# Optimization experiments

Hardware: AMD Instinct MI355X
Metric: run time of the kernel (lower is better)

## Reference

```python
import jax, jax.numpy as jnp
import numpy as np

L, B, C = 512, 64, 512  # seq_len, batch, tags_size


def setup_inputs() -> dict:
    key = jax.random.key(0)
    k1, k2, k3, k4, k5, k6 = jax.random.split(key, 6)
    std = (1.0 / C) ** 0.5
    emit = jax.random.normal(k1, (L, B, C), dtype=jnp.float32)
    trans = jax.random.normal(k2, (C, C), dtype=jnp.float32) * std
    trans_from_start = jax.random.normal(k3, (C,), dtype=jnp.float32) * std
    trans_to_end = jax.random.normal(k4, (C,), dtype=jnp.float32) * std
    target = jax.random.randint(k5, (L, B), 0, C)
    # left-aligned length mask so mask.sum(0)-1 indexes the last valid step
    lens = jax.random.randint(k6, (B,), L // 2, L + 1)
    mask = jnp.arange(L)[:, None] < lens[None, :]
    return {"emit": emit, "target": target, "mask": mask, "trans": trans,
            "trans_from_start": trans_from_start, "trans_to_end": trans_to_end}


def _log_z(emit, mask, trans, trans_from_start, trans_to_end):
    log_alpha0 = emit[0] + trans_from_start  # (B, C)

    def step(log_alpha, xs):
        e_i, m_i = xs  # (B, C), (B,)
        # scores[b, j] = logsumexp_i( log_alpha[b, i] + trans[i, j] + e_i[b, j] )
        s = jax.nn.logsumexp(log_alpha[:, :, None] + trans[None, :, :] + e_i[:, None, :], axis=1)
        log_alpha = jnp.where(m_i[:, None], s, log_alpha)
        return log_alpha, None

    log_alpha, _ = jax.lax.scan(step, log_alpha0, (emit[1:], mask[1:]))
    return jax.nn.logsumexp(log_alpha + trans_to_end, axis=1).sum()


def _score(emit, target, mask, trans, trans_from_start, trans_to_end):
    l, b, c = emit.shape
    tr = trans[target[:-1], target[1:]]  # (L-1, B)
    scores = jnp.concatenate([jnp.zeros((1, b), emit.dtype), tr], axis=0)
    scores = scores + jnp.take_along_axis(emit, target[:, :, None], axis=2)[..., 0]
    score = jnp.where(mask, scores, jnp.zeros((), emit.dtype)).sum()
    ends = mask.sum(axis=0) - 1  # (B,) index of last valid step
    last_tags = target[ends, jnp.arange(b)]
    score = score + trans_from_start[target[0]].sum() + trans_to_end[last_tags].sum()
    return score


def reference(emit, target, mask, trans, trans_from_start, trans_to_end):
    b = emit.shape[1]
    log_z = _log_z(emit, mask, trans, trans_from_start, trans_to_end)
    score = _score(emit, target, mask, trans, trans_from_start, trans_to_end)
    return (log_z - score) / b
```

## Files before the change

### kernel.cpp

```cpp
#include <hip/hip_runtime.h>
#include <hip/hip_bf16.h>
#include <stdint.h>

#define LL 512
#define BB 64
#define CC 512
#define TM 255

typedef float float4v __attribute__((ext_vector_type(4)));
typedef int   int4v   __attribute__((ext_vector_type(4)));
typedef int   int8v   __attribute__((ext_vector_type(8)));

#define WS_ET     262144
#define WS_SCORE  524288
#define WS_SVA    524292
#define WS_SVB    524548
#define WS_ALPHA  528384
#define WS_BETA   659456


__device__ __forceinline__ bool mask_at(const void* maskp, bool is_byte, int t, int b) {
    if (is_byte) return ((const unsigned char*)maskp)[t * BB + b] != 0;
    return ((const int*)maskp)[t * BB + b] != 0;
}

__device__ __forceinline__ float rowmax16_dpp(float x) {
    int t;
    t = __builtin_amdgcn_update_dpp(0, __float_as_int(x), 0x128, 0xF, 0xF, true);
    x = fmaxf(x, __int_as_float(t));
    t = __builtin_amdgcn_update_dpp(0, __float_as_int(x), 0x124, 0xF, 0xF, true);
    x = fmaxf(x, __int_as_float(t));
    t = __builtin_amdgcn_update_dpp(0, __float_as_int(x), 0x122, 0xF, 0xF, true);
    x = fmaxf(x, __int_as_float(t));
    t = __builtin_amdgcn_update_dpp(0, __float_as_int(x), 0x121, 0xF, 0xF, true);
    x = fmaxf(x, __int_as_float(t));
    return x;
}

__device__ __forceinline__ float4v vmax4(float4v a, float4v b) {
    float4v r;
    r[0] = fmaxf(a[0], b[0]); r[1] = fmaxf(a[1], b[1]);
    r[2] = fmaxf(a[2], b[2]); r[3] = fmaxf(a[3], b[3]);
    return r;
}
__device__ __forceinline__ float4v vmin4s(float4v a, float c) {
    float4v r;
    r[0] = fminf(a[0], c); r[1] = fminf(a[1], c);
    r[2] = fminf(a[2], c); r[3] = fminf(a[3], c);
    return r;
}

__device__ __forceinline__ void step_barrier() {
    asm volatile("s_waitcnt lgkmcnt(0)" ::: "memory");
    __builtin_amdgcn_sched_barrier(0);
    __builtin_amdgcn_s_barrier();
    asm volatile("" ::: "memory");
}

__global__ void prep_kernel(const float* __restrict__ trans, unsigned char* __restrict__ ws) {
    int g = blockIdx.x * blockDim.x + threadIdx.x;
    if (g == 0) *(float*)(ws + WS_SCORE) = 0.0f;
    if (g >= 512 * 128) return;
    int n  = g & 511;
    int pd = g >> 9;
    int wv = pd >> 4, rw = pd & 15;
    float f[4], ft[4];
#pragma unroll
    for (int nt = 0; nt < 4; ++nt) {
        int k = 64 * wv + 16 * nt + rw;
        f[nt]  = __expf(trans[(size_t)k * CC + n]);
        ft[nt] = __expf(trans[(size_t)n * CC + k]);
    }
    int r = 0;
    r = __builtin_amdgcn_cvt_pk_fp8_f32(f[0], f[1], r, false);
    r = __builtin_amdgcn_cvt_pk_fp8_f32(f[2], f[3], r, true);
    ((int*)ws)[n * 128 + pd] = r;
    int r2 = 0;
    r2 = __builtin_amdgcn_cvt_pk_fp8_f32(ft[0], ft[1], r2, false);
    r2 = __builtin_amdgcn_cvt_pk_fp8_f32(ft[2], ft[3], r2, true);
    ((int*)(ws + WS_ET))[n * 128 + pd] = r2;
}

__launch_bounds__(512, 2)
__global__ void crf_scan_kernel(const float* __restrict__ emit,
                                const int* __restrict__ target,
                                const void* __restrict__ maskp,
                                const float* __restrict__ trans,
                                const float* __restrict__ tfs,
                                const float* __restrict__ t2e,
                                unsigned char* __restrict__ ws) {
    const int tid = threadIdx.x;
    const bool is_byte = ((const unsigned char*)maskp)[1] != 0;

    if (blockIdx.x >= 8) {
        int sb = blockIdx.x - 8;
        float val = 0.0f;
        for (int e = sb * 512 + tid; e < LL * BB; e += 32 * 512) {
            int t = e >> 6, b = e & 63;
            if (mask_at(maskp, is_byte, t, b)) {
                int tg  = target[t * BB + b];
                float v = emit[(size_t)(t * BB + b) * CC + tg];
                if (t > 0) v += trans[(size_t)target[(t - 1) * BB + b] * CC + tg];
                val += v;
            }
        }
        if (sb == 0 && tid < BB) {
            int b = tid;
            val += tfs[target[b]];
            int lo = 0, hi = LL;
            while (lo < hi) {
                int mid = (lo + hi) >> 1;
                if (mask_at(maskp, is_byte, mid, b)) lo = mid + 1; else hi = mid;
            }
            val += t2e[target[(lo - 1) * BB + b]];
        }
        for (int off = 32; off > 0; off >>= 1) val += __shfl_down(val, off);
        if ((tid & 63) == 0) atomicAdd((float*)(ws + WS_SCORE), val);
        return;
    }

    const bool is_fwd = blockIdx.x < 4;
    const int B0 = (is_fwd ? blockIdx.x : blockIdx.x - 4) * 16;

    __shared__ __align__(16) unsigned char p8[2][16 * 528];
    __shared__ __align__(16) float mslot[4][16];
    __shared__ float m0S[16];
    __shared__ float red[16][32];
    __shared__ int   lenS[16];
    __shared__ float mInitS;

    const int wv   = tid >> 6;
    const int lane = tid & 63;
    const int q    = lane >> 4;
    const int r15  = lane & 15;

    const unsigned char* ews = ws + (is_fwd ? 0 : WS_ET);
    int8v ef[4][4];
#pragma unroll
    for (int nt = 0; nt < 4; ++nt) {
        int n = (wv * 4 + nt) * 16 + r15;
#pragma unroll
        for (int kk4 = 0; kk4 < 4; ++kk4) {
            const unsigned char* src = ews + n * 512 + kk4 * 128 + q * 32;
            int4v lo = *(const int4v*)(src);
            int4v hi = *(const int4v*)(src + 16);
            ef[nt][kk4] = __builtin_shufflevector(lo, hi, 0, 1, 2, 3, 4, 5, 6, 7);
        }
    }

    const int c5 = tid >> 5;
    const int s5 = tid & 31;

    if (is_fwd) {
        {
            float lmax = -3.0e38f;
#pragma unroll
            for (int i = 0; i < 4; ++i) {
                int j4 = s5 + 32 * i;
                float4v em = *(const float4v*)(emit + (size_t)(B0 + c5) * CC + 4 * j4);
                float4v tf = *(const float4v*)(tfs + 4 * j4);
                float4v a = em + tf;
                lmax = fmaxf(lmax, fmaxf(fmaxf(a.x, a.y), fmaxf(a.z, a.w)));
            }
            red[c5][s5] = lmax;
        }
        __syncthreads();
        if (tid < 16) {
            float m0 = red[tid][0];
            for (int s = 1; s < 32; ++s) m0 = fmaxf(m0, red[tid][s]);
            m0S[tid] = m0;
            mslot[0][tid] = 1.0f;
            mslot[1][tid] = 0.0f;
            mslot[2][tid] = 0.0f;
            mslot[3][tid] = 0.0f;
        }
        __syncthreads();
        {
            float m0 = m0S[c5];
#pragma unroll
            for (int i = 0; i < 4; ++i) {
                int pd = s5 + 32 * i;
                int wvv = pd >> 4, rw = pd & 15;
                float f[4];
#pragma unroll
                for (int nt = 0; nt < 4; ++nt) {
                    int k = 64 * wvv + 16 * nt + rw;
                    f[nt] = __expf(emit[(size_t)(B0 + c5) * CC + k] + tfs[k] - m0);
                }
                int r = 0;
                r = __builtin_amdgcn_cvt_pk_fp8_f32(f[0], f[1], r, false);
                r = __builtin_amdgcn_cvt_pk_fp8_f32(f[2], f[3], r, true);
                *(int*)(&p8[0][0] + c5 * 528 + pd * 4) = r;
            }
        }
        __syncthreads();
    } else {
        {
            float m = t2e[tid];
            for (int off = 32; off > 0; off >>= 1) m = fmaxf(m, __shfl_xor(m, off));
            if (lane == 0) ((float*)red)[wv] = m;
        }
        if (tid < 16) {
            mslot[0][tid] = 0.0f;
            mslot[1][tid] = 0.0f;
            mslot[2][tid] = 0.0f;
            mslot[3][tid] = 0.0f;
        }
        __syncthreads();
        if (tid == 0) {
            float m = ((float*)red)[0];
            for (int i = 1; i < 8; ++i) m = fmaxf(m, ((float*)red)[i]);
            mInitS = __expf(m);
        }
        __syncthreads();
        {
#pragma unroll
            for (int i = 0; i < 4; ++i) {
                int pd = s5 + 32 * i;
                int wvv = pd >> 4, rw = pd & 15;
                float f[4];
#pragma unroll
                for (int nt = 0; nt < 4; ++nt)
                    f[nt] = __expf(t2e[64 * wvv + 16 * nt + rw]);
                int r = 0;
                r = __builtin_amdgcn_cvt_pk_fp8_f32(f[0], f[1], r, false);
                r = __builtin_amdgcn_cvt_pk_fp8_f32(f[2], f[3], r, true);
                *(int*)(&p8[0][0] + c5 * 528 + pd * 4) = r;
                *(int*)(&p8[1][0] + c5 * 528 + pd * 4) = r;
            }
            int part = 0;
            for (int k = 0; k < 16; ++k)
                part += mask_at(maskp, is_byte, s5 * 16 + k, B0 + c5) ? 1 : 0;
            red[c5][s5] = (float)part;
        }
        __syncthreads();
        if (tid < 16) {
            int s = 0;
            for (int i = 0; i < 32; ++i) s += (int)red[tid][i];
            lenS[tid] = s;
        }
        __syncthreads();
    }

    int4v gsum = {0, 0, 0, 0};
    const float4v z4 = {0.f, 0.f, 0.f, 0.f};

    if (is_fwd) {
        const float* eb0 = emit + (size_t)(BB + B0 + q * 4) * CC + (wv * 64 + r15);
        const float* eb1 = eb0 + 2 * CC;
        float4v ex4[4];
#pragma unroll
        for (int nt = 0; nt < 4; ++nt) {
            ex4[nt][0] = __expf(eb0[0 * CC + nt * 16]);
            ex4[nt][1] = __expf(eb0[1 * CC + nt * 16]);
            ex4[nt][2] = __expf(eb1[0 * CC + nt * 16]);
            ex4[nt][3] = __expf(eb1[1 * CC + nt * 16]);
        }

#pragma unroll 2
        for (int t = 1; t <= TM; ++t) {
            const int wp = t & 1;
            const int rp = wp ^ 1;
            eb0 += BB * CC;
            eb1 += BB * CC;

            const unsigned char* pr = &p8[rp][0] + r15 * 528 + q * 32;
            int8v af[4];
#pragma unroll
            for (int kk4 = 0; kk4 < 4; ++kk4) {
                int4v lo = *(const int4v*)(pr + kk4 * 128);
                int4v hi = *(const int4v*)(pr + kk4 * 128 + 16);
                af[kk4] = __builtin_shufflevector(lo, hi, 0, 1, 2, 3, 4, 5, 6, 7);
            }
            int4v me = *(const int4v*)&mslot[(t - 1) & 3][q * 4];

            float4v emn4[4];
#pragma unroll
            for (int nt = 0; nt < 4; ++nt) {
                emn4[nt][0] = eb0[0 * CC + nt * 16];
                emn4[nt][1] = eb0[1 * CC + nt * 16];
                emn4[nt][2] = eb1[0 * CC + nt * 16];
                emn4[nt][3] = eb1[1 * CC + nt * 16];
            }

            int4v e4 = me >> 23;
            int4v s2b = (248 - e4) << 23;
            float4v s24;
            s24[0] = __int_as_float(s2b[0]); s24[1] = __int_as_float(s2b[1]);
            s24[2] = __int_as_float(s2b[2]); s24[3] = __int_as_float(s2b[3]);

            if (wv == 0 && r15 == 0)
                *(float4v*)&mslot[(t + 1) & 3][q * 4] = z4;

            float4v acc[4];
#pragma unroll
            for (int nt = 0; nt < 4; ++nt) acc[nt] = z4;

#pragma unroll
            for (int kk4 = 0; kk4 < 4; ++kk4)
#pragma unroll
                for (int nt = 0; nt < 2; ++nt)
                    acc[nt] = __builtin_amdgcn_mfma_scale_f32_16x16x128_f8f6f4(
                        af[kk4], ef[nt][kk4], acc[nt],
                        0, 0, 0, 0x7F7F7F7F, 0, 0x7F7F7F7F);

            float4v exn4[4];
#pragma unroll
            for (int nt = 0; nt < 4; ++nt) {
                exn4[nt][0] = __expf(emn4[nt][0]);
                exn4[nt][1] = __expf(emn4[nt][1]);
                exn4[nt][2] = __expf(emn4[nt][2]);
                exn4[nt][3] = __expf(emn4[nt][3]);
            }

#pragma unroll
            for (int kk4 = 0; kk4 < 4; ++kk4)
#pragma unroll
                for (int nt = 2; nt < 4; ++nt)
                    acc[nt] = __builtin_amdgcn_mfma_scale_f32_16x16x128_f8f6f4(
                        af[kk4], ef[nt][kk4], acc[nt],
                        0, 0, 0, 0x7F7F7F7F, 0, 0x7F7F7F7F);

            float4v p4[4];
#pragma unroll
            for (int nt = 0; nt < 4; ++nt) {
                float4v exr = ex4[nt] * s24;
                p4[nt] = acc[nt] * exr;
            }

            if (t == TM) {
                float* wA = (float*)(ws + WS_ALPHA) + (size_t)(B0 + q * 4) * CC + (wv * 64 + r15);
#pragma unroll
                for (int nt = 0; nt < 4; ++nt)
#pragma unroll
                    for (int rr = 0; rr < 4; ++rr)
                        wA[(size_t)rr * CC + nt * 16] = p4[nt][rr];
            }

            float4v rm4 = vmax4(vmax4(p4[0], p4[1]), vmax4(p4[2], p4[3]));
#pragma unroll
            for (int rr = 0; rr < 4; ++rr) {
                float mr = rowmax16_dpp(rm4[rr]);
                if (r15 == 0)
                    atomicMax((int*)&mslot[t & 3][q * 4 + rr], __float_as_int(mr));
            }

            {
                unsigned char* wrow = &p8[wp][0] + (wv * 16 + r15) * 4;
                float4v pc[4];
#pragma unroll
                for (int nt = 0; nt < 4; ++nt) pc[nt] = vmin4s(p4[nt], 448.0f);
#pragma unroll
                for (int rr = 0; rr < 4; ++rr) {
                    int r = 0;
                    r = __builtin_amdgcn_cvt_pk_fp8_f32(pc[0][rr], pc[1][rr], r, false);
                    r = __builtin_amdgcn_cvt_pk_fp8_f32(pc[2][rr], pc[3][rr], r, true);
                    *(int*)(wrow + (q * 4 + rr) * 528) = r;
                }
            }

            if (wv == 0 && r15 == 0) gsum += (e4 - 121);

#pragma unroll
            for (int nt = 0; nt < 4; ++nt) ex4[nt] = exn4[nt];
            step_barrier();
        }
        if (wv == 0 && r15 == 0) {
#pragma unroll
            for (int rr = 0; rr < 4; ++rr)
                ((float*)(ws + WS_SVA))[B0 + q * 4 + rr] =
                    m0S[q * 4 + rr] + 0.6931471805599453f * (float)gsum[rr];
        }
    } else {
        int lenR[4];
#pragma unroll
        for (int rr = 0; rr < 4; ++rr) lenR[rr] = lenS[q * 4 + rr];
        const int eInit = __float_as_int(mInitS) >> 23;

        const float* eb0 = emit + ((size_t)(LL - 1) * BB + B0 + q * 4) * CC + (wv * 64 + r15);
        const float* eb1 = eb0 + 2 * CC;
        float4v ex4[4];
#pragma unroll
        for (int nt = 0; nt < 4; ++nt) {
            ex4[nt][0] = __expf(eb0[0 * CC + nt * 16]);
            ex4[nt][1] = __expf(eb0[1 * CC + nt * 16]);
            ex4[nt][2] = __expf(eb1[0 * CC + nt * 16]);
            ex4[nt][3] = __expf(eb1[1 * CC + nt * 16]);
        }

#pragma unroll 2
        for (int it = 0; it < 256; ++it) {
            const int t  = 510 - it;
            const int wp = it & 1;
            const int rp = wp ^ 1;
            eb0 -= BB * CC;
            eb1 -= BB * CC;

            const unsigned char* pr = &p8[rp][0] + r15 * 528 + q * 32;
            int8v af[4];
#pragma unroll
            for (int kk4 = 0; kk4 < 4; ++kk4) {
                int4v lo = *(const int4v*)(pr + kk4 * 128);
                int4v hi = *(const int4v*)(pr + kk4 * 128 + 16);
                af[kk4] = __builtin_shufflevector(lo, hi, 0, 1, 2, 3, 4, 5, 6, 7);
            }
            int4v me = *(const int4v*)&mslot[(it + 3) & 3][q * 4];

            float4v emn4[4];
#pragma unroll
            for (int nt = 0; nt < 4; ++nt) {
                emn4[nt][0] = eb0[0 * CC + nt * 16];
                emn4[nt][1] = eb0[1 * CC + nt * 16];
                emn4[nt][2] = eb1[0 * CC + nt * 16];
                emn4[nt][3] = eb1[1 * CC + nt * 16];
            }

            int4v e4 = me >> 23;
            int4v eU;
            float4v s2U;
#pragma unroll
            for (int rr = 0; rr < 4; ++rr) {
                bool ui = (t >= lenR[rr] - 2);
                int e = ui ? eInit : e4[rr];
                eU[rr] = e;
                s2U[rr] = __int_as_float((248 - e) << 23);
            }

            if (wv == 0 && r15 == 0)
                *(float4v*)&mslot[(it + 1) & 3][q * 4] = z4;

            float4v acc[4];
#pragma unroll
            for (int nt = 0; nt < 4; ++nt) acc[nt] = z4;

#pragma unroll
            for (int kk4 = 0; kk4 < 4; ++kk4)
#pragma unroll
                for (int nt = 0; nt < 2; ++nt)
                    acc[nt] = __builtin_amdgcn_mfma_scale_f32_16x16x128_f8f6f4(
                        af[kk4], ef[nt][kk4], acc[nt],
                        0, 0, 0, 0x7F7F7F7F, 0, 0x7F7F7F7F);

            float4v exn4[4];
#pragma unroll
            for (int nt = 0; nt < 4; ++nt) {
                exn4[nt][0] = __expf(emn4[nt][0]);
                exn4[nt][1] = __expf(emn4[nt][1]);
                exn4[nt][2] = __expf(emn4[nt][2]);
                exn4[nt][3] = __expf(emn4[nt][3]);
            }

#pragma unroll
            for (int kk4 = 0; kk4 < 4; ++kk4)
#pragma unroll
                for (int nt = 2; nt < 4; ++nt)
                    acc[nt] = __builtin_amdgcn_mfma_scale_f32_16x16x128_f8f6f4(
                        af[kk4], ef[nt][kk4], acc[nt],
                        0, 0, 0, 0x7F7F7F7F, 0, 0x7F7F7F7F);

            float4v p4[4];
#pragma unroll
            for (int nt = 0; nt < 4; ++nt) {
                float4v exr = ex4[nt] * s2U;
                p4[nt] = acc[nt] * exr;
            }

            if (t == TM) {
                float* wB = (float*)(ws + WS_BETA) + (size_t)(B0 + q * 4) * CC + (wv * 64 + r15);
#pragma unroll
                for (int nt = 0; nt < 4; ++nt) {
                    float e2 = __expf(t2e[wv * 64 + nt * 16 + r15]);
#pragma unroll
                    for (int rr = 0; rr < 4; ++rr)
                        wB[(size_t)rr * CC + nt * 16] = (t <= lenR[rr] - 2) ? p4[nt][rr] : e2;
                }
            }

            float4v rm4 = vmax4(vmax4(p4[0], p4[1]), vmax4(p4[2], p4[3]));
#pragma unroll
            for (int rr = 0; rr < 4; ++rr) {
                float mr = rowmax16_dpp(rm4[rr]);
                if (r15 == 0)
                    atomicMax((int*)&mslot[it & 3][q * 4 + rr], __float_as_int(mr));
            }

            {
                unsigned char* wrow = &p8[wp][0] + (wv * 16 + r15) * 4;
                float4v pc[4];
#pragma unroll
                for (int nt = 0; nt < 4; ++nt) pc[nt] = vmin4s(p4[nt], 448.0f);
#pragma unroll
                for (int rr = 0; rr < 4; ++rr) {
                    int r = 0;
                    r = __builtin_amdgcn_cvt_pk_fp8_f32(pc[0][rr], pc[1][rr], r, false);
                    r = __builtin_amdgcn_cvt_pk_fp8_f32(pc[2][rr], pc[3][rr], r, true);
                    if (t <= lenR[rr] - 2)
                        *(int*)(wrow + (q * 4 + rr) * 528) = r;
                }
            }

            if (wv == 0 && r15 == 0) {
#pragma unroll
                for (int rr = 0; rr < 4; ++rr)
                    if (t <= lenR[rr] - 2) gsum[rr] += (eU[rr] - 121);
            }

#pragma unroll
            for (int nt = 0; nt < 4; ++nt) ex4[nt] = exn4[nt];
            step_barrier();
        }
        if (wv == 0 && r15 == 0) {
#pragma unroll
            for (int rr = 0; rr < 4; ++rr)
                ((float*)(ws + WS_SVB))[B0 + q * 4 + rr] =
                    0.6931471805599453f * (float)gsum[rr];
        }
    }
}

__global__ void combine_kernel(const unsigned char* __restrict__ ws, float* __restrict__ out) {
    __shared__ float acc8[8];
    const int tid = threadIdx.x;
    const int c  = tid >> 3;
    const int s8 = tid & 7;
    const float* A = (const float*)(ws + WS_ALPHA) + (size_t)c * CC;
    const float* B = (const float*)(ws + WS_BETA)  + (size_t)c * CC;
    float d = 0.0f;
    for (int i = s8; i < CC; i += 8) d += A[i] * B[i];
    d += __shfl_xor(d, 1);
    d += __shfl_xor(d, 2);
    d += __shfl_xor(d, 4);
    float v = 0.0f;
    if (s8 == 0)
        v = ((const float*)(ws + WS_SVA))[c] + ((const float*)(ws + WS_SVB))[c] + __logf(d);
    for (int off = 32; off > 0; off >>= 1) v += __shfl_down(v, off);
    if ((tid & 63) == 0) acc8[tid >> 6] = v;
    __syncthreads();
    if (tid == 0) {
        float s = 0.0f;
        for (int i = 0; i < 8; ++i) s += acc8[i];
        out[0] = (s - *(const float*)(ws + WS_SCORE)) * (1.0f / 64.0f);
    }
}

extern "C" void kernel_launch(void* const* d_in, const int* in_sizes, int n_in,
                              void* d_out, int out_size, void* d_ws, size_t ws_size,
                              hipStream_t stream) {
    const float* emit   = (const float*)d_in[0];
    const int*   target = (const int*)d_in[1];
    const void*  maskp  = d_in[2];
    const float* trans  = (const float*)d_in[3];
    const float* tfs    = (const float*)d_in[4];
    const float* t2e    = (const float*)d_in[5];
    unsigned char* ws   = (unsigned char*)d_ws;
    float* out          = (float*)d_out;

    prep_kernel<<<256, 256, 0, stream>>>(trans, ws);
    crf_scan_kernel<<<40, 512, 0, stream>>>(emit, target, maskp, trans, tfs, t2e, ws);
    combine_kernel<<<1, 512, 0, stream>>>(ws, out);
}
```

Measured before the change: 495.4 us.

## Fuse trans prep into scan kernel and interleave MFMA halves with epilogue

```diff
diff --git a/kernel.cpp b/kernel.cpp
--- a/kernel.cpp
+++ b/kernel.cpp
@@ -11,13 +11,16 @@
 typedef int   int4v   __attribute__((ext_vector_type(4)));
 typedef int   int8v   __attribute__((ext_vector_type(8)));
 
-#define WS_ET     262144
-#define WS_SCORE  524288
-#define WS_SVA    524292
-#define WS_SVB    524548
+#define WS_SPART  524288
+#define WS_SVA    524416
+#define WS_SVB    524672
 #define WS_ALPHA  528384
 #define WS_BETA   659456
 
+
+__device__ __forceinline__ int kperm(int p) {
+    return 64 * (p >> 6) + 16 * (p & 3) + ((p >> 2) & 15);
+}
 
 __device__ __forceinline__ bool mask_at(const void* maskp, bool is_byte, int t, int b) {
     if (is_byte) return ((const unsigned char*)maskp)[t * BB + b] != 0;
@@ -37,48 +40,11 @@
     return x;
 }
 
-__device__ __forceinline__ float4v vmax4(float4v a, float4v b) {
-    float4v r;
-    r[0] = fmaxf(a[0], b[0]); r[1] = fmaxf(a[1], b[1]);
-    r[2] = fmaxf(a[2], b[2]); r[3] = fmaxf(a[3], b[3]);
-    return r;
-}
-__device__ __forceinline__ float4v vmin4s(float4v a, float c) {
-    float4v r;
-    r[0] = fminf(a[0], c); r[1] = fminf(a[1], c);
-    r[2] = fminf(a[2], c); r[3] = fminf(a[3], c);
-    return r;
-}
-
 __device__ __forceinline__ void step_barrier() {
     asm volatile("s_waitcnt lgkmcnt(0)" ::: "memory");
     __builtin_amdgcn_sched_barrier(0);
     __builtin_amdgcn_s_barrier();
     asm volatile("" ::: "memory");
-}
-
-__global__ void prep_kernel(const float* __restrict__ trans, unsigned char* __restrict__ ws) {
-    int g = blockIdx.x * blockDim.x + threadIdx.x;
-    if (g == 0) *(float*)(ws + WS_SCORE) = 0.0f;
-    if (g >= 512 * 128) return;
-    int n  = g & 511;
-    int pd = g >> 9;
-    int wv = pd >> 4, rw = pd & 15;
-    float f[4], ft[4];
-#pragma unroll
-    for (int nt = 0; nt < 4; ++nt) {
-        int k = 64 * wv + 16 * nt + rw;
-        f[nt]  = __expf(trans[(size_t)k * CC + n]);
-        ft[nt] = __expf(trans[(size_t)n * CC + k]);
-    }
-    int r = 0;
-    r = __builtin_amdgcn_cvt_pk_fp8_f32(f[0], f[1], r, false);
-    r = __builtin_amdgcn_cvt_pk_fp8_f32(f[2], f[3], r, true);
-    ((int*)ws)[n * 128 + pd] = r;
-    int r2 = 0;
-    r2 = __builtin_amdgcn_cvt_pk_fp8_f32(ft[0], ft[1], r2, false);
-    r2 = __builtin_amdgcn_cvt_pk_fp8_f32(ft[2], ft[3], r2, true);
-    ((int*)(ws + WS_ET))[n * 128 + pd] = r2;
 }
 
 __launch_bounds__(512, 2)
@@ -93,6 +59,7 @@
     const bool is_byte = ((const unsigned char*)maskp)[1] != 0;
 
     if (blockIdx.x >= 8) {
+        __shared__ float sred[8];
         int sb = blockIdx.x - 8;
         float val = 0.0f;
         for (int e = sb * 512 + tid; e < LL * BB; e += 32 * 512) {
@@ -115,7 +82,13 @@
             val += t2e[target[(lo - 1) * BB + b]];
         }
         for (int off = 32; off > 0; off >>= 1) val += __shfl_down(val, off);
-        if ((tid & 63) == 0) atomicAdd((float*)(ws + WS_SCORE), val);
+        if ((tid & 63) == 0) sred[tid >> 6] = val;
+        __syncthreads();
+        if (tid == 0) {
+            float s = 0.0f;
+            for (int i = 0; i < 8; ++i) s += sred[i];
+            ((float*)(ws + WS_SPART))[sb] = s;
+        }
         return;
     }
 
@@ -134,17 +107,36 @@
     const int q    = lane >> 4;
     const int r15  = lane & 15;
 
-    const unsigned char* ews = ws + (is_fwd ? 0 : WS_ET);
     int8v ef[4][4];
 #pragma unroll
     for (int nt = 0; nt < 4; ++nt) {
         int n = (wv * 4 + nt) * 16 + r15;
 #pragma unroll
         for (int kk4 = 0; kk4 < 4; ++kk4) {
-            const unsigned char* src = ews + n * 512 + kk4 * 128 + q * 32;
-            int4v lo = *(const int4v*)(src);
-            int4v hi = *(const int4v*)(src + 16);
-            ef[nt][kk4] = __builtin_shufflevector(lo, hi, 0, 1, 2, 3, 4, 5, 6, 7);
+            int pb = kk4 * 128 + q * 32;
+            int8v v;
+#pragma unroll
+            for (int d = 0; d < 8; ++d) {
+                int p0 = pb + (d & 3) * 4 + (d >> 2) * 16;
+                int kb = 64 * (p0 >> 6) + ((p0 >> 2) & 15);
+                float f0, f1, f2, f3;
+                if (is_fwd) {
+                    f0 = __expf(trans[(size_t)(kb +  0) * CC + n]);
+                    f1 = __expf(trans[(size_t)(kb + 16) * CC + n]);
+                    f2 = __expf(trans[(size_t)(kb + 32) * CC + n]);
+                    f3 = __expf(trans[(size_t)(kb + 48) * CC + n]);
+                } else {
+                    f0 = __expf(trans[(size_t)n * CC + kb +  0]);
+                    f1 = __expf(trans[(size_t)n * CC + kb + 16]);
+                    f2 = __expf(trans[(size_t)n * CC + kb + 32]);
+                    f3 = __expf(trans[(size_t)n * CC + kb + 48]);
+                }
+                int r = 0;
+                r = __builtin_amdgcn_cvt_pk_fp8_f32(f0, f1, r, false);
+                r = __builtin_amdgcn_cvt_pk_fp8_f32(f2, f3, r, true);
+                v[d] = r;
+            }
+            ef[nt][kk4] = v;
         }
     }
 
@@ -244,6 +236,7 @@
 
     int4v gsum = {0, 0, 0, 0};
     const float4v z4 = {0.f, 0.f, 0.f, 0.f};
+    const float4v c448 = 448.0f;
 
     if (is_fwd) {
         const float* eb0 = emit + (size_t)(BB + B0 + q * 4) * CC + (wv * 64 + r15);
@@ -292,77 +285,90 @@
             if (wv == 0 && r15 == 0)
                 *(float4v*)&mslot[(t + 1) & 3][q * 4] = z4;
 
-            float4v acc[4];
-#pragma unroll
-            for (int nt = 0; nt < 4; ++nt) acc[nt] = z4;
-
-#pragma unroll
-            for (int kk4 = 0; kk4 < 4; ++kk4)
-#pragma unroll
-                for (int nt = 0; nt < 2; ++nt)
-                    acc[nt] = __builtin_amdgcn_mfma_scale_f32_16x16x128_f8f6f4(
-                        af[kk4], ef[nt][kk4], acc[nt],
-                        0, 0, 0, 0x7F7F7F7F, 0, 0x7F7F7F7F);
-
-            float4v exn4[4];
-#pragma unroll
-            for (int nt = 0; nt < 4; ++nt) {
-                exn4[nt][0] = __expf(emn4[nt][0]);
-                exn4[nt][1] = __expf(emn4[nt][1]);
-                exn4[nt][2] = __expf(emn4[nt][2]);
-                exn4[nt][3] = __expf(emn4[nt][3]);
-            }
-
-#pragma unroll
-            for (int kk4 = 0; kk4 < 4; ++kk4)
-#pragma unroll
-                for (int nt = 2; nt < 4; ++nt)
-                    acc[nt] = __builtin_amdgcn_mfma_scale_f32_16x16x128_f8f6f4(
-                        af[kk4], ef[nt][kk4], acc[nt],
-                        0, 0, 0, 0x7F7F7F7F, 0, 0x7F7F7F7F);
-
-            float4v p4[4];
-#pragma unroll
-            for (int nt = 0; nt < 4; ++nt) {
-                float4v exr = ex4[nt] * s24;
-                p4[nt] = acc[nt] * exr;
+            float4v acc0 = z4, acc1 = z4, acc2 = z4, acc3 = z4;
+
+            __builtin_amdgcn_s_setprio(1);
+#pragma unroll
+            for (int kk4 = 0; kk4 < 4; ++kk4) {
+                acc0 = __builtin_amdgcn_mfma_scale_f32_16x16x128_f8f6f4(
+                    af[kk4], ef[0][kk4], acc0, 0, 0, 0, 0x7F7F7F7F, 0, 0x7F7F7F7F);
+                acc1 = __builtin_amdgcn_mfma_scale_f32_16x16x128_f8f6f4(
+                    af[kk4], ef[1][kk4], acc1, 0, 0, 0, 0x7F7F7F7F, 0, 0x7F7F7F7F);
+            }
+            __builtin_amdgcn_s_setprio(0);
+
+            float4v p0 = acc0 * (ex4[0] * s24);
+            float4v p1 = acc1 * (ex4[1] * s24);
+            float4v rmA = __builtin_elementwise_max(p0, p1);
+#pragma unroll
+            for (int rr = 0; rr < 4; ++rr) {
+                float mr = rowmax16_dpp(rmA[rr]);
+                if (r15 == 0)
+                    atomicMax((int*)&mslot[t & 3][q * 4 + rr], __float_as_int(mr));
+            }
+            float4v pA0 = __builtin_elementwise_min(p0, c448);
+            float4v pA1 = __builtin_elementwise_min(p1, c448);
+            int rlo[4];
+#pragma unroll
+            for (int rr = 0; rr < 4; ++rr)
+                rlo[rr] = __builtin_amdgcn_cvt_pk_fp8_f32(pA0[rr], pA1[rr], 0, false);
+
+            float4v exn0, exn1;
+            exn0[0] = __expf(emn4[0][0]); exn0[1] = __expf(emn4[0][1]);
+            exn0[2] = __expf(emn4[0][2]); exn0[3] = __expf(emn4[0][3]);
+            exn1[0] = __expf(emn4[1][0]); exn1[1] = __expf(emn4[1][1]);
+            exn1[2] = __expf(emn4[1][2]); exn1[3] = __expf(emn4[1][3]);
+
+            __builtin_amdgcn_s_setprio(1);
+#pragma unroll
+            for (int kk4 = 0; kk4 < 4; ++kk4) {
+                acc2 = __builtin_amdgcn_mfma_scale_f32_16x16x128_f8f6f4(
+                    af[kk4], ef[2][kk4], acc2, 0, 0, 0, 0x7F7F7F7F, 0, 0x7F7F7F7F);
+                acc3 = __builtin_amdgcn_mfma_scale_f32_16x16x128_f8f6f4(
+                    af[kk4], ef[3][kk4], acc3, 0, 0, 0, 0x7F7F7F7F, 0, 0x7F7F7F7F);
+            }
+            __builtin_amdgcn_s_setprio(0);
+
+            float4v exn2, exn3;
+            exn2[0] = __expf(emn4[2][0]); exn2[1] = __expf(emn4[2][1]);
+            exn2[2] = __expf(emn4[2][2]); exn2[3] = __expf(emn4[2][3]);
+            exn3[0] = __expf(emn4[3][0]); exn3[1] = __expf(emn4[3][1]);
+            exn3[2] = __expf(emn4[3][2]); exn3[3] = __expf(emn4[3][3]);
+
+            float4v p2 = acc2 * (ex4[2] * s24);
+            float4v p3 = acc3 * (ex4[3] * s24);
+            float4v rmB = __builtin_elementwise_max(p2, p3);
+#pragma unroll
+            for (int rr = 0; rr < 4; ++rr) {
+                float mr = rowmax16_dpp(rmB[rr]);
+                if (r15 == 0)
+                    atomicMax((int*)&mslot[t & 3][q * 4 + rr], __float_as_int(mr));
+            }
+            float4v pB0 = __builtin_elementwise_min(p2, c448);
+            float4v pB1 = __builtin_elementwise_min(p3, c448);
+            {
+                unsigned char* wrow = &p8[wp][0] + (wv * 16 + r15) * 4;
+#pragma unroll
+                for (int rr = 0; rr < 4; ++rr) {
+                    int r = __builtin_amdgcn_cvt_pk_fp8_f32(pB0[rr], pB1[rr], rlo[rr], true);
+                    *(int*)(wrow + (q * 4 + rr) * 528) = r;
+                }
             }
 
             if (t == TM) {
                 float* wA = (float*)(ws + WS_ALPHA) + (size_t)(B0 + q * 4) * CC + (wv * 64 + r15);
 #pragma unroll
-                for (int nt = 0; nt < 4; ++nt)
-#pragma unroll
-                    for (int rr = 0; rr < 4; ++rr)
-                        wA[(size_t)rr * CC + nt * 16] = p4[nt][rr];
-            }
-
-            float4v rm4 = vmax4(vmax4(p4[0], p4[1]), vmax4(p4[2], p4[3]));
-#pragma unroll
-            for (int rr = 0; rr < 4; ++rr) {
-                float mr = rowmax16_dpp(rm4[rr]);
-                if (r15 == 0)
-                    atomicMax((int*)&mslot[t & 3][q * 4 + rr], __float_as_int(mr));
-            }
-
-            {
-                unsigned char* wrow = &p8[wp][0] + (wv * 16 + r15) * 4;
-                float4v pc[4];
-#pragma unroll
-                for (int nt = 0; nt < 4; ++nt) pc[nt] = vmin4s(p4[nt], 448.0f);
-#pragma unroll
                 for (int rr = 0; rr < 4; ++rr) {
-                    int r = 0;
-                    r = __builtin_amdgcn_cvt_pk_fp8_f32(pc[0][rr], pc[1][rr], r, false);
-                    r = __builtin_amdgcn_cvt_pk_fp8_f32(pc[2][rr], pc[3][rr], r, true);
-                    *(int*)(wrow + (q * 4 + rr) * 528) = r;
+                    wA[(size_t)rr * CC +  0] = p0[rr];
+                    wA[(size_t)rr * CC + 16] = p1[rr];
+                    wA[(size_t)rr * CC + 32] = p2[rr];
+                    wA[(size_t)rr * CC + 48] = p3[rr];
                 }
             }
 
-            if (wv == 0 && r15 == 0) gsum += (e4 - 121);
-
-#pragma unroll
-            for (int nt = 0; nt < 4; ++nt) ex4[nt] = exn4[nt];
+            gsum += (e4 - 121);
+
+            ex4[0] = exn0; ex4[1] = exn1; ex4[2] = exn2; ex4[3] = exn3;
             step_barrier();
         }
         if (wv == 0 && r15 == 0) {
@@ -376,6 +382,12 @@
 #pragma unroll
         for (int rr = 0; rr < 4; ++rr) lenR[rr] = lenS[q * 4 + rr];
         const int eInit = __float_as_int(mInitS) >> 23;
+
+        int rInit = 0;
+        rInit = __builtin_amdgcn_cvt_pk_fp8_f32(__expf(t2e[64 * wv + r15]),
+                                                __expf(t2e[64 * wv + 16 + r15]), rInit, false);
+        rInit = __builtin_amdgcn_cvt_pk_fp8_f32(__expf(t2e[64 * wv + 32 + r15]),
+                                                __expf(t2e[64 * wv + 48 + r15]), rInit, true);
 
         const float* eb0 = emit + ((size_t)(LL - 1) * BB + B0 + q * 4) * CC + (wv * 64 + r15);
         const float* eb1 = eb0 + 2 * CC;
@@ -418,9 +430,11 @@
             int4v e4 = me >> 23;
             int4v eU;
             float4v s2U;
+            bool live[4];
 #pragma unroll
             for (int rr = 0; rr < 4; ++rr) {
                 bool ui = (t >= lenR[rr] - 2);
+                live[rr] = !ui;
                 int e = ui ? eInit : e4[rr];
                 eU[rr] = e;
                 s2U[rr] = __int_as_float((248 - e) << 23);
@@ -429,40 +443,75 @@
             if (wv == 0 && r15 == 0)
                 *(float4v*)&mslot[(it + 1) & 3][q * 4] = z4;
 
-            float4v acc[4];
-#pragma unroll
-            for (int nt = 0; nt < 4; ++nt) acc[nt] = z4;
-
-#pragma unroll
-            for (int kk4 = 0; kk4 < 4; ++kk4)
-#pragma unroll
-                for (int nt = 0; nt < 2; ++nt)
-                    acc[nt] = __builtin_amdgcn_mfma_scale_f32_16x16x128_f8f6f4(
-                        af[kk4], ef[nt][kk4], acc[nt],
-                        0, 0, 0, 0x7F7F7F7F, 0, 0x7F7F7F7F);
-
-            float4v exn4[4];
-#pragma unroll
-            for (int nt = 0; nt < 4; ++nt) {
-                exn4[nt][0] = __expf(emn4[nt][0]);
-                exn4[nt][1] = __expf(emn4[nt][1]);
-                exn4[nt][2] = __expf(emn4[nt][2]);
-                exn4[nt][3] = __expf(emn4[nt][3]);
-            }
-
-#pragma unroll
-            for (int kk4 = 0; kk4 < 4; ++kk4)
-#pragma unroll
-                for (int nt = 2; nt < 4; ++nt)
-                    acc[nt] = __builtin_amdgcn_mfma_scale_f32_16x16x128_f8f6f4(
-                        af[kk4], ef[nt][kk4], acc[nt],
-                        0, 0, 0, 0x7F7F7F7F, 0, 0x7F7F7F7F);
-
-            float4v p4[4];
-#pragma unroll
-            for (int nt = 0; nt < 4; ++nt) {
-                float4v exr = ex4[nt] * s2U;
-                p4[nt] = acc[nt] * exr;
+            float4v acc0 = z4, acc1 = z4, acc2 = z4, acc3 = z4;
+
+            __builtin_amdgcn_s_setprio(1);
+#pragma unroll
+            for (int kk4 = 0; kk4 < 4; ++kk4) {
+                acc0 = __builtin_amdgcn_mfma_scale_f32_16x16x128_f8f6f4(
+                    af[kk4], ef[0][kk4], acc0, 0, 0, 0, 0x7F7F7F7F, 0, 0x7F7F7F7F);
+                acc1 = __builtin_amdgcn_mfma_scale_f32_16x16x128_f8f6f4(
+                    af[kk4], ef[1][kk4], acc1, 0, 0, 0, 0x7F7F7F7F, 0, 0x7F7F7F7F);
+            }
+            __builtin_amdgcn_s_setprio(0);
+
+            float4v p0 = acc0 * (ex4[0] * s2U);
+            float4v p1 = acc1 * (ex4[1] * s2U);
+            float4v rmA = __builtin_elementwise_max(p0, p1);
+#pragma unroll
+            for (int rr = 0; rr < 4; ++rr) {
+                float mr = rowmax16_dpp(rmA[rr]);
+                if (r15 == 0)
+                    atomicMax((int*)&mslot[it & 3][q * 4 + rr], __float_as_int(mr));
+            }
+            float4v pA0 = __builtin_elementwise_min(p0, c448);
+            float4v pA1 = __builtin_elementwise_min(p1, c448);
+            int rlo[4];
+#pragma unroll
+            for (int rr = 0; rr < 4; ++rr)
+                rlo[rr] = __builtin_amdgcn_cvt_pk_fp8_f32(pA0[rr], pA1[rr], 0, false);
+
+            float4v exn0, exn1;
+            exn0[0] = __expf(emn4[0][0]); exn0[1] = __expf(emn4[0][1]);
+            exn0[2] = __expf(emn4[0][2]); exn0[3] = __expf(emn4[0][3]);
+            exn1[0] = __expf(emn4[1][0]); exn1[1] = __expf(emn4[1][1]);
+            exn1[2] = __expf(emn4[1][2]); exn1[3] = __expf(emn4[1][3]);
+
+            __builtin_amdgcn_s_setprio(1);
+#pragma unroll
+            for (int kk4 = 0; kk4 < 4; ++kk4) {
+                acc2 = __builtin_amdgcn_mfma_scale_f32_16x16x128_f8f6f4(
+                    af[kk4], ef[2][kk4], acc2, 0, 0, 0, 0x7F7F7F7F, 0, 0x7F7F7F7F);
+                acc3 = __builtin_amdgcn_mfma_scale_f32_16x16x128_f8f6f4(
+                    af[kk4], ef[3][kk4], acc3, 0, 0, 0, 0x7F7F7F7F, 0, 0x7F7F7F7F);
+            }
+            __builtin_amdgcn_s_setprio(0);
+
+            float4v exn2, exn3;
+            exn2[0] = __expf(emn4[2][0]); exn2[1] = __expf(emn4[2][1]);
+            exn2[2] = __expf(emn4[2][2]); exn2[3] = __expf(emn4[2][3]);
+            exn3[0] = __expf(emn4[3][0]); exn3[1] = __expf(emn4[3][1]);
+            exn3[2] = __expf(emn4[3][2]); exn3[3] = __expf(emn4[3][3]);
+
+            float4v p2 = acc2 * (ex4[2] * s2U);
+            float4v p3 = acc3 * (ex4[3] * s2U);
+            float4v rmB = __builtin_elementwise_max(p2, p3);
+#pragma unroll
+            for (int rr = 0; rr < 4; ++rr) {
+                float mr = rowmax16_dpp(rmB[rr]);
+                if (r15 == 0)
+                    atomicMax((int*)&mslot[it & 3][q * 4 + rr], __float_as_int(mr));
+            }
+            float4v pB0 = __builtin_elementwise_min(p2, c448);
+            float4v pB1 = __builtin_elementwise_min(p3, c448);
+            {
+                unsigned char* wrow = &p8[wp][0] + (wv * 16 + r15) * 4;
+#pragma unroll
+                for (int rr = 0; rr < 4; ++rr) {
+                    int r = __builtin_amdgcn_cvt_pk_fp8_f32(pB0[rr], pB1[rr], rlo[rr], true);
+                    int rs = live[rr] ? r : rInit;
+                    *(int*)(wrow + (q * 4 + rr) * 528) = rs;
+                }
             }
 
             if (t == TM) {
@@ -470,43 +519,18 @@
 #pragma unroll
                 for (int nt = 0; nt < 4; ++nt) {
                     float e2 = __expf(t2e[wv * 64 + nt * 16 + r15]);
+                    float4v* psel = (nt == 0) ? &p0 : (nt == 1) ? &p1 : (nt == 2) ? &p2 : &p3;
 #pragma unroll
                     for (int rr = 0; rr < 4; ++rr)
-                        wB[(size_t)rr * CC + nt * 16] = (t <= lenR[rr] - 2) ? p4[nt][rr] : e2;
+                        wB[(size_t)rr * CC + nt * 16] = live[rr] ? (*psel)[rr] : e2;
                 }
             }
 
-            float4v rm4 = vmax4(vmax4(p4[0], p4[1]), vmax4(p4[2], p4[3]));
-#pragma unroll
-            for (int rr = 0; rr < 4; ++rr) {
-                float mr = rowmax16_dpp(rm4[rr]);
-                if (r15 == 0)
-                    atomicMax((int*)&mslot[it & 3][q * 4 + rr], __float_as_int(mr));
-            }
-
-            {
-                unsigned char* wrow = &p8[wp][0] + (wv * 16 + r15) * 4;
-                float4v pc[4];
-#pragma unroll
-                for (int nt = 0; nt < 4; ++nt) pc[nt] = vmin4s(p4[nt], 448.0f);
-#pragma unroll
-                for (int rr = 0; rr < 4; ++rr) {
-                    int r = 0;
-                    r = __builtin_amdgcn_cvt_pk_fp8_f32(pc[0][rr], pc[1][rr], r, false);
-                    r = __builtin_amdgcn_cvt_pk_fp8_f32(pc[2][rr], pc[3][rr], r, true);
-                    if (t <= lenR[rr] - 2)
-                        *(int*)(wrow + (q * 4 + rr) * 528) = r;
-                }
-            }
-
-            if (wv == 0 && r15 == 0) {
-#pragma unroll
-                for (int rr = 0; rr < 4; ++rr)
-                    if (t <= lenR[rr] - 2) gsum[rr] += (eU[rr] - 121);
-            }
-
-#pragma unroll
-            for (int nt = 0; nt < 4; ++nt) ex4[nt] = exn4[nt];
+#pragma unroll
+            for (int rr = 0; rr < 4; ++rr)
+                gsum[rr] += live[rr] ? (eU[rr] - 121) : 0;
+
+            ex4[0] = exn0; ex4[1] = exn1; ex4[2] = exn2; ex4[3] = exn3;
             step_barrier();
         }
         if (wv == 0 && r15 == 0) {
@@ -539,7 +563,9 @@
     if (tid == 0) {
         float s = 0.0f;
         for (int i = 0; i < 8; ++i) s += acc8[i];
-        out[0] = (s - *(const float*)(ws + WS_SCORE)) * (1.0f / 64.0f);
+        float sc = 0.0f;
+        for (int i = 0; i < 32; ++i) sc += ((const float*)(ws + WS_SPART))[i];
+        out[0] = (s - sc) * (1.0f / 64.0f);
     }
 }
 
@@ -555,7 +581,6 @@
     unsigned char* ws   = (unsigned char*)d_ws;
     float* out          = (float*)d_out;
 
-    prep_kernel<<<256, 256, 0, stream>>>(trans, ws);
     crf_scan_kernel<<<40, 512, 0, stream>>>(emit, target, maskp, trans, tfs, t2e, ws);
     combine_kernel<<<1, 512, 0, stream>>>(ws, out);
 }
```

New measurement: 714.0 us. 1.44x slower.
